# Optimization experiments

Hardware: AMD Instinct MI355X
Metric: run time of the kernel (lower is better)

The kernel has to match this reference:

```python
import jax, jax.numpy as jnp
import numpy as np

B, N, D = 8, 1024, 1024
H = 16
HD = D // H  # 64
SCALE = float(HD) ** -0.5


def setup_inputs() -> dict:
    key = jax.random.key(0)
    k1, k2, k3 = jax.random.split(key, 3)
    x = jax.random.normal(k1, (B, N, D), dtype=jnp.float32)
    W_qkv = jax.random.normal(k2, (D, 3 * D), dtype=jnp.float32) * (D ** -0.5)
    b_qkv = jnp.zeros((3 * D,), dtype=jnp.float32)
    W_o = jax.random.normal(k3, (D, D), dtype=jnp.float32) * (D ** -0.5)
    b_o = jnp.zeros((D,), dtype=jnp.float32)
    return {"x": x, "W_qkv": W_qkv, "b_qkv": b_qkv, "W_o": W_o, "b_o": b_o}


def reference(x, W_qkv, b_qkv, W_o, b_o):
    b, n, _ = x.shape
    qkv = x @ W_qkv + b_qkv                      # (B, N, 3D)
    qkv = qkv.reshape(b, n, H, 3 * HD).transpose(0, 2, 1, 3)  # (B, H, N, 3*HD)
    q, k, v = jnp.split(qkv, 3, axis=-1)          # each (B, H, N, HD)
    attn = jnp.einsum('bhnd,bhmd->bhnm', q, k) * SCALE
    attn = jax.nn.softmax(attn, axis=-1)          # (B, H, N, N); dropout p=0 -> identity
    heads = jnp.einsum('bhnm,bhmd->bhnd', attn, v)
    heads = heads.transpose(0, 2, 1, 3).reshape(b, n, H * HD)  # (B, N, D)
    return heads @ W_o + b_o
```

## Files before the change

### kernel.cpp

```cpp
#include <hip/hip_runtime.h>
#include <hip/hip_bf16.h>

typedef unsigned short ushort_t;
typedef __bf16 bf16x8 __attribute__((ext_vector_type(8)));
typedef float floatx4 __attribute__((ext_vector_type(4)));

#define MFMA(a, b, c) __builtin_amdgcn_mfma_f32_16x16x32_bf16(a, b, c, 0, 0, 0)

__device__ __forceinline__ ushort_t f2b(float f) {
    union { ushort_t u; __bf16 h; } cvt; cvt.h = (__bf16)f; return cvt.u;
}

__device__ __forceinline__ void async_copy16(const ushort_t* g, ushort_t* l) {
    __builtin_amdgcn_global_load_lds(
        (const __attribute__((address_space(1))) void*)g,
        (__attribute__((address_space(3))) void*)l, 16, 0, 0);
}

__global__ void prep(const float* __restrict__ xin, ushort_t* __restrict__ xb,
                     const float* __restrict__ Wqkv, ushort_t* __restrict__ WqkvT,
                     const float* __restrict__ Wo, ushort_t* __restrict__ WoT) {
    __shared__ float tile[32][33];
    int bb = blockIdx.x;
    if (bb < 4096) {
        int i = bb * 256 + threadIdx.x;
        const float4* xf = (const float4*)xin;
        float4 a = xf[i * 2], b = xf[i * 2 + 1];
        union { ushort_t s[8]; uint4 v; } p;
        p.s[0] = f2b(a.x); p.s[1] = f2b(a.y); p.s[2] = f2b(a.z); p.s[3] = f2b(a.w);
        p.s[4] = f2b(b.x); p.s[5] = f2b(b.y); p.s[6] = f2b(b.z); p.s[7] = f2b(b.w);
        ((uint4*)xb)[i] = p.v;
    } else if (bb < 7168) {
        int b2 = bb - 4096;
        int p0 = (b2 % 96) * 32, k0 = (b2 / 96) * 32;
        int which = p0 >> 10, rem = p0 & 1023;
        int n0 = (rem >> 6) * 192 + which * 64 + (rem & 63);
        int tx = threadIdx.x & 31, ty = threadIdx.x >> 5;
#pragma unroll
        for (int i = 0; i < 4; ++i)
            tile[ty + i * 8][tx] = Wqkv[(size_t)(k0 + ty + i * 8) * 3072 + n0 + tx];
        __syncthreads();
#pragma unroll
        for (int i = 0; i < 4; ++i)
            WqkvT[(size_t)(p0 + ty + i * 8) * 1024 + k0 + tx] = f2b(tile[tx][ty + i * 8]);
    } else {
        int b3 = bb - 7168;
        int n0 = (b3 & 31) * 32, k0 = (b3 >> 5) * 32;
        int tx = threadIdx.x & 31, ty = threadIdx.x >> 5;
#pragma unroll
        for (int i = 0; i < 4; ++i)
            tile[ty + i * 8][tx] = Wo[(size_t)(k0 + ty + i * 8) * 1024 + n0 + tx];
        __syncthreads();
#pragma unroll
        for (int i = 0; i < 4; ++i)
            WoT[(size_t)(n0 + ty + i * 8) * 1024 + k0 + tx] = f2b(tile[tx][ty + i * 8]);
    }
}

__device__ __forceinline__ int tswz(int n, int m) {
    return n * 128 + (((m >> 3) ^ (n & 15)) << 3) + (m & 7);
}

__global__ __launch_bounds__(256, 4) void gemm_qkv(
    const ushort_t* __restrict__ A,
    const ushort_t* __restrict__ Bt,
    const float* __restrict__ bias,
    ushort_t* __restrict__ Qb, ushort_t* __restrict__ Kb, ushort_t* __restrict__ Vtb) {
    const int K = 1024;
    __shared__ __align__(16) ushort_t SH[16384];
    ushort_t* Alds = SH;
    ushort_t* Blds = SH + 8192;
    int tid = threadIdx.x;
    int wave = tid >> 6, lane = tid & 63;
    int quad = lane >> 4, l16 = lane & 15;
    int wm = (wave >> 1) * 64, wn = (wave & 1) * 64;
    int m0 = blockIdx.x * 128, n0 = blockIdx.y * 128;

    floatx4 acc[4][4] = {};

    int srow[4], scol[4];
#pragma unroll
    for (int p = 0; p < 4; ++p) {
        int slot = (wave * 4 + p) * 64 + lane;
        int row = slot >> 3;
        srow[p] = row;
        scol[p] = ((slot & 7) ^ (row & 7)) * 8;
    }

    for (int kt = 0; kt < 16; ++kt) {
        int k0 = kt * 64;
        __syncthreads();
#pragma unroll
        for (int p = 0; p < 4; ++p) {
            int t = wave * 4 + p;
            async_copy16(&A[(m0 + srow[p]) * K + k0 + scol[p]], &Alds[t * 512]);
            async_copy16(&Bt[(n0 + srow[p]) * K + k0 + scol[p]], &Blds[t * 512]);
        }
        __syncthreads();
#pragma unroll
        for (int ki = 0; ki < 2; ++ki) {
            bf16x8 af[4], bfv[4];
            int sc = ((ki * 4 + quad) ^ (l16 & 7)) * 8;
#pragma unroll
            for (int i = 0; i < 4; ++i) {
                __builtin_memcpy(&af[i],  &Alds[(wm + i * 16 + l16) * 64 + sc], 16);
                __builtin_memcpy(&bfv[i], &Blds[(wn + i * 16 + l16) * 64 + sc], 16);
            }
#pragma unroll
            for (int i = 0; i < 4; ++i)
#pragma unroll
                for (int j = 0; j < 4; ++j)
                    acc[i][j] = MFMA(af[i], bfv[j], acc[i][j]);
        }
    }

    int which = n0 >> 10;
    int b = m0 >> 10;

    if (which < 2) {
        ushort_t* dst = which ? Kb : Qb;
        float sc = which ? 1.0f : 0.18033688f;
#pragma unroll
        for (int j = 0; j < 4; ++j) {
            int C = n0 + wn + j * 16 + l16;
            int c = C & 1023;
            int h = c >> 6, d = c & 63;
            float bv = bias[((C >> 6) & 15) * 192 + which * 64 + (C & 63)];
            size_t hb = (size_t)(b * 16 + h) * 65536 + d;
#pragma unroll
            for (int i = 0; i < 4; ++i)
#pragma unroll
                for (int g = 0; g < 4; ++g) {
                    int n_tok = (m0 & 1023) + wm + i * 16 + quad * 4 + g;
                    dst[hb + (size_t)n_tok * 64] = f2b((acc[i][j][g] + bv) * sc);
                }
        }
    } else {
        __syncthreads();
#pragma unroll
        for (int j = 0; j < 4; ++j) {
            int C = n0 + wn + j * 16 + l16;
            int nl2 = wn + j * 16 + l16;
            float bv = bias[((C >> 6) & 15) * 192 + 128 + (C & 63)];
#pragma unroll
            for (int i = 0; i < 4; ++i)
#pragma unroll
                for (int g = 0; g < 4; ++g) {
                    int ml = wm + i * 16 + quad * 4 + g;
                    SH[tswz(nl2, ml)] = f2b(acc[i][j][g] + bv);
                }
        }
        __syncthreads();
        int r = tid >> 1, half = tid & 1;
        int vcol = (n0 - 2048) + r;
        int h = vcol >> 6, d = vcol & 63;
        size_t base = ((size_t)(b * 16 + h) * 64 + d) * 1024 + (m0 & 1023) + half * 64;
#pragma unroll
        for (int i8 = 0; i8 < 8; ++i8) {
            int chunk = half * 8 + i8;
            uint4 v;
            __builtin_memcpy(&v, &SH[r * 128 + ((chunk ^ (r & 15)) << 3)], 16);
            __builtin_memcpy(&Vtb[base + i8 * 8], &v, 16);
        }
    }
}

__global__ __launch_bounds__(256, 4) void attn(
    const ushort_t* __restrict__ Qb, const ushort_t* __restrict__ Kb,
    const ushort_t* __restrict__ Vtb, ushort_t* __restrict__ heads) {
    __shared__ __align__(16) ushort_t Klds[4096];
    __shared__ __align__(16) ushort_t Vlds[4096];
    __shared__ __align__(16) ushort_t Plds[128 * 76];
    int tid = threadIdx.x;
    int wave = tid >> 6, lane = tid & 63;
    int quad = lane >> 4, l16 = lane & 15;

    int slot = blockIdx.y + 16 * blockIdx.z;
    int bh = blockIdx.x + 8 * (slot >> 3);
    int qx = slot & 7;
    int b = bh >> 4, h = bh & 15;
    const ushort_t* Qh = Qb + (size_t)bh * 65536;
    const ushort_t* Kh = Kb + (size_t)bh * 65536;
    const ushort_t* Vh = Vtb + (size_t)bh * 65536;

    bf16x8 qa[2][2];
#pragma unroll
    for (int mi = 0; mi < 2; ++mi) {
        int qrow = qx * 128 + wave * 32 + mi * 16 + l16;
        __builtin_memcpy(&qa[mi][0], &Qh[qrow * 64 + quad * 8], 16);
        __builtin_memcpy(&qa[mi][1], &Qh[qrow * 64 + 32 + quad * 8], 16);
    }

    floatx4 oacc[2][4] = {};
    floatx4 oext[2] = {};

    bf16x8 onesfrag;
    {
        ushort_t v = (l16 == 0) ? (ushort_t)0x3F80 : (ushort_t)0;
        ushort_t tmp[8] = {v, v, v, v, v, v, v, v};
        __builtin_memcpy(&onesfrag, tmp, 16);
    }

    int srow[2], scol[2];
#pragma unroll
    for (int p = 0; p < 2; ++p) {
        int slot2 = (wave * 2 + p) * 64 + lane;
        int row = slot2 >> 3;
        srow[p] = row;
        scol[p] = ((slot2 & 7) ^ (row & 7)) * 8;
    }

    for (int kt = 0; kt < 16; ++kt) {
        int k0 = kt * 64;
        __syncthreads();
#pragma unroll
        for (int p = 0; p < 2; ++p) {
            int t = wave * 2 + p;
            async_copy16(&Kh[(k0 + srow[p]) * 64 + scol[p]], &Klds[t * 512]);
            async_copy16(&Vh[srow[p] * 1024 + k0 + scol[p]], &Vlds[t * 512]);
        }
        __syncthreads();

        bf16x8 kf[4][2];
#pragma unroll
        for (int n = 0; n < 4; ++n)
#pragma unroll
            for (int ki = 0; ki < 2; ++ki) {
                int sc = ((ki * 4 + quad) ^ (l16 & 7)) * 8;
                __builtin_memcpy(&kf[n][ki], &Klds[(n * 16 + l16) * 64 + sc], 16);
            }
#pragma unroll
        for (int mi = 0; mi < 2; ++mi) {
            int prow = wave * 32 + mi * 16 + l16;
#pragma unroll
            for (int n = 0; n < 4; ++n) {
                floatx4 z = {0.f, 0.f, 0.f, 0.f};
#pragma unroll
                for (int ki = 0; ki < 2; ++ki)
                    z = MFMA(kf[n][ki], qa[mi][ki], z);
                union { ushort_t s[4]; double d8; } pk;
#pragma unroll
                for (int g = 0; g < 4; ++g)
                    pk.s[g] = f2b(__builtin_exp2f(z[g]));
                __builtin_memcpy(
                    &Plds[prow * 76 + n * 16 + quad * 4], &pk, 8);
            }
        }

        bf16x8 vf[4][2];
#pragma unroll
        for (int n = 0; n < 4; ++n)
#pragma unroll
            for (int ki = 0; ki < 2; ++ki) {
                int sc = ((ki * 4 + quad) ^ (l16 & 7)) * 8;
                __builtin_memcpy(&vf[n][ki], &Vlds[(n * 16 + l16) * 64 + sc], 16);
            }
#pragma unroll
        for (int mi = 0; mi < 2; ++mi) {
            bf16x8 pa[2];
            int prow = wave * 32 + mi * 16 + l16;
#pragma unroll
            for (int ki = 0; ki < 2; ++ki)
                __builtin_memcpy(&pa[ki], &Plds[prow * 76 + ki * 32 + quad * 8], 16);
            __builtin_amdgcn_s_setprio(1);
#pragma unroll
            for (int n = 0; n < 4; ++n)
#pragma unroll
                for (int ki = 0; ki < 2; ++ki)
                    oacc[mi][n] = MFMA(pa[ki], vf[n][ki], oacc[mi][n]);
#pragma unroll
            for (int ki = 0; ki < 2; ++ki)
                oext[mi] = MFMA(pa[ki], onesfrag, oext[mi]);
            __builtin_amdgcn_s_setprio(0);
        }
    }

#pragma unroll
    for (int mi = 0; mi < 2; ++mi)
#pragma unroll
        for (int g = 0; g < 4; ++g) {
            float l = __shfl(oext[mi][g], (lane & 48));
            float inv = 1.f / l;
            int n_tok = qx * 128 + wave * 32 + mi * 16 + quad * 4 + g;
#pragma unroll
            for (int n = 0; n < 4; ++n)
                heads[(size_t)(b * 1024 + n_tok) * 1024 + h * 64 + n * 16 + l16] =
                    f2b(oacc[mi][n][g] * inv);
        }
}

__global__ __launch_bounds__(256, 4) void gemm_out(
    const ushort_t* __restrict__ A,
    const ushort_t* __restrict__ Bt,
    const float* __restrict__ bias,
    float* __restrict__ out) {
    const int K = 1024;
    __shared__ __align__(16) ushort_t Alds[128 * 64];
    __shared__ __align__(16) ushort_t Blds[128 * 64];
    int tid = threadIdx.x;
    int wave = tid >> 6, lane = tid & 63;
    int quad = lane >> 4, l16 = lane & 15;
    int wm = (wave >> 1) * 64, wn = (wave & 1) * 64;
    int m0 = blockIdx.x * 128, n0 = blockIdx.y * 128;

    floatx4 acc[4][4] = {};

    int srow[4], scol[4];
#pragma unroll
    for (int p = 0; p < 4; ++p) {
        int slot = (wave * 4 + p) * 64 + lane;
        int row = slot >> 3;
        srow[p] = row;
        scol[p] = ((slot & 7) ^ (row & 7)) * 8;
    }

    for (int kt = 0; kt < 16; ++kt) {
        int k0 = kt * 64;
        __syncthreads();
#pragma unroll
        for (int p = 0; p < 4; ++p) {
            int t = wave * 4 + p;
            async_copy16(&A[(m0 + srow[p]) * K + k0 + scol[p]], &Alds[t * 512]);
            async_copy16(&Bt[(n0 + srow[p]) * K + k0 + scol[p]], &Blds[t * 512]);
        }
        __syncthreads();
#pragma unroll
        for (int ki = 0; ki < 2; ++ki) {
            bf16x8 af[4], bfv[4];
            int sc = ((ki * 4 + quad) ^ (l16 & 7)) * 8;
#pragma unroll
            for (int i = 0; i < 4; ++i) {
                __builtin_memcpy(&af[i],  &Alds[(wm + i * 16 + l16) * 64 + sc], 16);
                __builtin_memcpy(&bfv[i], &Blds[(wn + i * 16 + l16) * 64 + sc], 16);
            }
#pragma unroll
            for (int i = 0; i < 4; ++i)
#pragma unroll
                for (int j = 0; j < 4; ++j)
                    acc[i][j] = MFMA(af[i], bfv[j], acc[i][j]);
        }
    }

#pragma unroll
    for (int j = 0; j < 4; ++j) {
        int C = n0 + wn + j * 16 + l16;
        float bv = bias[C];
#pragma unroll
        for (int i = 0; i < 4; ++i)
#pragma unroll
            for (int g = 0; g < 4; ++g) {
                int R = m0 + wm + i * 16 + quad * 4 + g;
                out[(size_t)R * 1024 + C] = acc[i][j][g] + bv;
            }
    }
}

extern "C" void kernel_launch(void* const* d_in, const int* in_sizes, int n_in,
                              void* d_out, int out_size, void* d_ws, size_t ws_size,
                              hipStream_t stream) {
    const float* x    = (const float*)d_in[0];
    const float* Wqkv = (const float*)d_in[1];
    const float* bqkv = (const float*)d_in[2];
    const float* Wo   = (const float*)d_in[3];
    const float* bo   = (const float*)d_in[4];

    char* ws = (char*)d_ws;
    const size_t MB = 1u << 20;
    ushort_t* xb    = (ushort_t*)(ws);
    ushort_t* Qb    = (ushort_t*)(ws + 16 * MB);
    ushort_t* Kb    = (ushort_t*)(ws + 32 * MB);
    ushort_t* Vtb   = (ushort_t*)(ws + 48 * MB);
    ushort_t* WqkvT = (ushort_t*)(ws + 64 * MB);
    ushort_t* WoT   = (ushort_t*)(ws + 70 * MB);
    ushort_t* heads = (ushort_t*)(ws);

    prep<<<8192, 256, 0, stream>>>(x, xb, Wqkv, WqkvT, Wo, WoT);
    gemm_qkv<<<dim3(64, 24), 256, 0, stream>>>(xb, WqkvT, bqkv, Qb, Kb, Vtb);
    attn<<<dim3(8, 16, 8), 256, 0, stream>>>(Qb, Kb, Vtb, heads);
    gemm_out<<<dim3(64, 8), 256, 0, stream>>>(heads, WoT, bo, (float*)d_out);
}
```

Baseline: 230.3 us.

## Shrink attention tiles to 64 queries and 32 keys per block for occupancy

The attention kernel now gives each block 64 query rows (one 16-row MFMA tile per wave) and steps through keys in chunks of 32 instead of 64. It doubles the grid and raises launch bounds to 8 blocks per CU, with smaller LDS buffers and a new swizzled V layout. The aim is more resident waves to hide latency from the exp and the LDS round trip. In exchange, each K/V tile is loaded by twice as many blocks, and every block needs twice as many loop iterations and barriers, each with less MFMA work.

```diff
diff --git a/kernel.cpp b/kernel.cpp
--- a/kernel.cpp
+++ b/kernel.cpp
@@ -165,34 +165,31 @@
     }
 }
 
-__global__ __launch_bounds__(256, 4) void attn(
+__global__ __launch_bounds__(256, 8) void attn(
     const ushort_t* __restrict__ Qb, const ushort_t* __restrict__ Kb,
     const ushort_t* __restrict__ Vtb, ushort_t* __restrict__ heads) {
-    __shared__ __align__(16) ushort_t Klds[4096];
-    __shared__ __align__(16) ushort_t Vlds[4096];
-    __shared__ __align__(16) ushort_t Plds[128 * 76];
+    __shared__ __align__(16) ushort_t Klds[2048];
+    __shared__ __align__(16) ushort_t Vlds[2048];
+    __shared__ __align__(16) ushort_t Plds[64 * 38];
     int tid = threadIdx.x;
     int wave = tid >> 6, lane = tid & 63;
     int quad = lane >> 4, l16 = lane & 15;
 
     int slot = blockIdx.y + 16 * blockIdx.z;
-    int bh = blockIdx.x + 8 * (slot >> 3);
-    int qx = slot & 7;
+    int bh = blockIdx.x + 8 * (slot >> 4);
+    int qx = slot & 15;
     int b = bh >> 4, h = bh & 15;
     const ushort_t* Qh = Qb + (size_t)bh * 65536;
     const ushort_t* Kh = Kb + (size_t)bh * 65536;
     const ushort_t* Vh = Vtb + (size_t)bh * 65536;
 
-    bf16x8 qa[2][2];
-#pragma unroll
-    for (int mi = 0; mi < 2; ++mi) {
-        int qrow = qx * 128 + wave * 32 + mi * 16 + l16;
-        __builtin_memcpy(&qa[mi][0], &Qh[qrow * 64 + quad * 8], 16);
-        __builtin_memcpy(&qa[mi][1], &Qh[qrow * 64 + 32 + quad * 8], 16);
-    }
-
-    floatx4 oacc[2][4] = {};
-    floatx4 oext[2] = {};
+    int qrow = qx * 64 + wave * 16 + l16;
+    bf16x8 qa0, qa1;
+    __builtin_memcpy(&qa0, &Qh[qrow * 64 + quad * 8], 16);
+    __builtin_memcpy(&qa1, &Qh[qrow * 64 + 32 + quad * 8], 16);
+
+    floatx4 oacc[4] = {};
+    floatx4 oext = {};
 
     bf16x8 onesfrag;
     {
@@ -201,92 +198,68 @@
         __builtin_memcpy(&onesfrag, tmp, 16);
     }
 
-    int srow[2], scol[2];
-#pragma unroll
-    for (int p = 0; p < 2; ++p) {
-        int slot2 = (wave * 2 + p) * 64 + lane;
-        int row = slot2 >> 3;
-        srow[p] = row;
-        scol[p] = ((slot2 & 7) ^ (row & 7)) * 8;
-    }
-
-    for (int kt = 0; kt < 16; ++kt) {
-        int k0 = kt * 64;
-        __syncthreads();
-#pragma unroll
-        for (int p = 0; p < 2; ++p) {
-            int t = wave * 2 + p;
-            async_copy16(&Kh[(k0 + srow[p]) * 64 + scol[p]], &Klds[t * 512]);
-            async_copy16(&Vh[srow[p] * 1024 + k0 + scol[p]], &Vlds[t * 512]);
-        }
-        __syncthreads();
-
-        bf16x8 kf[4][2];
+    int krow = tid >> 3;
+    int kcol = ((tid & 7) ^ (krow & 7)) * 8;
+    int vj   = tid >> 3;
+    int vcp  = (tid & 7) ^ (vj & 7);
+    int vd   = 2 * vj + (vcp >> 2);
+    int vkc  = (vcp & 3) * 8;
+
+    int prow38 = (wave * 16 + l16) * 38;
+    int vhalf  = l16 & 1;
+    int vjlow  = l16 >> 1;
+    int vc0    = quad | (vhalf << 2);
+    int scK0   = (quad ^ (l16 & 7)) * 8;
+    int scK1   = ((4 + quad) ^ (l16 & 7)) * 8;
+
+    for (int kt = 0; kt < 32; ++kt) {
+        int k0 = kt * 32;
+        __syncthreads();
+        async_copy16(&Kh[(k0 + krow) * 64 + kcol], &Klds[wave * 512]);
+        async_copy16(&Vh[vd * 1024 + k0 + vkc], &Vlds[wave * 512]);
+        __syncthreads();
+
+#pragma unroll
+        for (int n = 0; n < 2; ++n) {
+            bf16x8 kf0, kf1;
+            __builtin_memcpy(&kf0, &Klds[(n * 16 + l16) * 64 + scK0], 16);
+            __builtin_memcpy(&kf1, &Klds[(n * 16 + l16) * 64 + scK1], 16);
+            floatx4 z = {0.f, 0.f, 0.f, 0.f};
+            z = MFMA(kf0, qa0, z);
+            z = MFMA(kf1, qa1, z);
+            union { ushort_t s[4]; double d8; } pk;
+#pragma unroll
+            for (int g = 0; g < 4; ++g)
+                pk.s[g] = f2b(__builtin_exp2f(z[g]));
+            __builtin_memcpy(&Plds[prow38 + n * 16 + quad * 4], &pk, 8);
+        }
+
+        bf16x8 pa;
+        __builtin_memcpy(&pa, &Plds[prow38 + quad * 8], 16);
+
+        __builtin_amdgcn_s_setprio(1);
+#pragma unroll
+        for (int n = 0; n < 4; ++n) {
+            int j = n * 8 + vjlow;
+            int c = (vc0 ^ (j & 7)) * 8;
+            bf16x8 vf;
+            __builtin_memcpy(&vf, &Vlds[j * 64 + c], 16);
+            oacc[n] = MFMA(pa, vf, oacc[n]);
+        }
+        oext = MFMA(pa, onesfrag, oext);
+        __builtin_amdgcn_s_setprio(0);
+    }
+
+#pragma unroll
+    for (int g = 0; g < 4; ++g) {
+        float l = __shfl(oext[g], (lane & 48));
+        float inv = 1.f / l;
+        int n_tok = qx * 64 + wave * 16 + quad * 4 + g;
 #pragma unroll
         for (int n = 0; n < 4; ++n)
-#pragma unroll
-            for (int ki = 0; ki < 2; ++ki) {
-                int sc = ((ki * 4 + quad) ^ (l16 & 7)) * 8;
-                __builtin_memcpy(&kf[n][ki], &Klds[(n * 16 + l16) * 64 + sc], 16);
-            }
-#pragma unroll
-        for (int mi = 0; mi < 2; ++mi) {
-            int prow = wave * 32 + mi * 16 + l16;
-#pragma unroll
-            for (int n = 0; n < 4; ++n) {
-                floatx4 z = {0.f, 0.f, 0.f, 0.f};
-#pragma unroll
-                for (int ki = 0; ki < 2; ++ki)
-                    z = MFMA(kf[n][ki], qa[mi][ki], z);
-                union { ushort_t s[4]; double d8; } pk;
-#pragma unroll
-                for (int g = 0; g < 4; ++g)
-                    pk.s[g] = f2b(__builtin_exp2f(z[g]));
-                __builtin_memcpy(
-                    &Plds[prow * 76 + n * 16 + quad * 4], &pk, 8);
-            }
-        }
-
-        bf16x8 vf[4][2];
-#pragma unroll
-        for (int n = 0; n < 4; ++n)
-#pragma unroll
-            for (int ki = 0; ki < 2; ++ki) {
-                int sc = ((ki * 4 + quad) ^ (l16 & 7)) * 8;
-                __builtin_memcpy(&vf[n][ki], &Vlds[(n * 16 + l16) * 64 + sc], 16);
-            }
-#pragma unroll
-        for (int mi = 0; mi < 2; ++mi) {
-            bf16x8 pa[2];
-            int prow = wave * 32 + mi * 16 + l16;
-#pragma unroll
-            for (int ki = 0; ki < 2; ++ki)
-                __builtin_memcpy(&pa[ki], &Plds[prow * 76 + ki * 32 + quad * 8], 16);
-            __builtin_amdgcn_s_setprio(1);
-#pragma unroll
-            for (int n = 0; n < 4; ++n)
-#pragma unroll
-                for (int ki = 0; ki < 2; ++ki)
-                    oacc[mi][n] = MFMA(pa[ki], vf[n][ki], oacc[mi][n]);
-#pragma unroll
-            for (int ki = 0; ki < 2; ++ki)
-                oext[mi] = MFMA(pa[ki], onesfrag, oext[mi]);
-            __builtin_amdgcn_s_setprio(0);
-        }
-    }
-
-#pragma unroll
-    for (int mi = 0; mi < 2; ++mi)
-#pragma unroll
-        for (int g = 0; g < 4; ++g) {
-            float l = __shfl(oext[mi][g], (lane & 48));
-            float inv = 1.f / l;
-            int n_tok = qx * 128 + wave * 32 + mi * 16 + quad * 4 + g;
-#pragma unroll
-            for (int n = 0; n < 4; ++n)
-                heads[(size_t)(b * 1024 + n_tok) * 1024 + h * 64 + n * 16 + l16] =
-                    f2b(oacc[mi][n][g] * inv);
-        }
+            heads[(size_t)(b * 1024 + n_tok) * 1024 + h * 64 + n * 16 + l16] =
+                f2b(oacc[n][g] * inv);
+    }
 }
 
 __global__ __launch_bounds__(256, 4) void gemm_out(
@@ -376,6 +349,6 @@
 
     prep<<<8192, 256, 0, stream>>>(x, xb, Wqkv, WqkvT, Wo, WoT);
     gemm_qkv<<<dim3(64, 24), 256, 0, stream>>>(xb, WqkvT, bqkv, Qb, Kb, Vtb);
-    attn<<<dim3(8, 16, 8), 256, 0, stream>>>(Qb, Kb, Vtb, heads);
+    attn<<<dim3(8, 16, 16), 256, 0, stream>>>(Qb, Kb, Vtb, heads);
     gemm_out<<<dim3(64, 8), 256, 0, stream>>>(heads, WoT, bo, (float*)d_out);
 }
```

New measurement: 236.7 us. 1.03x slower.
